# Performance work log

Hardware: AMD Instinct MI355X
Metric: run time of the kernel (lower is better)

The kernel has to match this reference:

```python
import jax, jax.numpy as jnp
import numpy as np

N = 100000        # nodes
E = 1600000       # edges (avg in-degree 16)
D_IN = 128
H = 4             # num_heads
D = 16            # out_feats per head
NEG_SLOPE = 0.2


def setup_inputs() -> dict:
    key = jax.random.key(0)
    k1, k2, k3, k4, k5 = jax.random.split(key, 5)
    feat = jax.random.normal(k1, (N, D_IN), dtype=jnp.float32)
    src = jax.random.randint(k2, (E,), 0, N, dtype=jnp.int32)
    dst = jax.random.randint(k3, (E,), 0, N, dtype=jnp.int32)
    # learned parameters (xavier-ish scale)
    W = jax.random.normal(k4, (H * D, D_IN), dtype=jnp.float32) * (2.0 / np.sqrt(D_IN + H * D))
    attn_weights = jax.random.normal(k5, (2 * H * D,), dtype=jnp.float32) * 0.1
    bias = jnp.zeros((H * D,), dtype=jnp.float32)
    return {"feat": feat, "src": src, "dst": dst, "W": W,
            "attn_weights": attn_weights, "bias": bias}


def reference(feat, src, dst, W, attn_weights, bias):
    # linear projection: [N, H*D] -> [N, H, D]
    z = (feat @ W.T).reshape(N, H, D)
    a = attn_weights.reshape(2, H, D)
    # per-node attention logits for source/destination roles: [N, H]
    el = jnp.einsum('nhd,hd->nh', z, a[0])
    er = jnp.einsum('nhd,hd->nh', z, a[1])
    # per-edge logits + LeakyReLU: [E, H]
    e = jax.nn.leaky_relu(el[src] + er[dst], NEG_SLOPE)
    # segment softmax over incoming edges of each destination node
    m = jax.ops.segment_max(e, dst, num_segments=N)        # [N, H]
    m = jnp.where(jnp.isfinite(m), m, 0.0)                 # guard isolated nodes
    ex = jnp.exp(e - m[dst])                               # [E, H]
    denom = jax.ops.segment_sum(ex, dst, num_segments=N)   # [N, H]
    denom = jnp.where(denom > 0, denom, 1.0)
    alpha = ex / denom[dst]                                # [E, H]
    # weighted scatter-aggregate: out[dst] += alpha * z[src]
    out = jax.ops.segment_sum(alpha[:, :, None] * z[src], dst, num_segments=N)
    return out + bias.reshape(H, D)
```

## Files before the change

### kernel.cpp

```cpp
#include <hip/hip_runtime.h>
#include <hip/hip_fp16.h>
#include <math.h>

#define NUM_H 4
#define HD 64
#define DIN 128
#define NEG_SLOPE 0.2f
#define LOG2E 1.4426950408889634f

#define NBK 128
#define BSH 10
#define NCH 256
#define SRCB 17

typedef _Float16 half8 __attribute__((ext_vector_type(8)));
typedef float f32x4 __attribute__((ext_vector_type(4)));

__device__ inline half8 pack8(float4 a, float4 b) {
  half8 h;
  h[0] = (_Float16)a.x; h[1] = (_Float16)a.y;
  h[2] = (_Float16)a.z; h[3] = (_Float16)a.w;
  h[4] = (_Float16)b.x; h[5] = (_Float16)b.y;
  h[6] = (_Float16)b.z; h[7] = (_Float16)b.w;
  return h;
}

__global__ __launch_bounds__(256) void k_proj(
    const float* __restrict__ feat, const float* __restrict__ Wm,
    const float* __restrict__ attn, __half* __restrict__ zh,
    float* __restrict__ el, float* __restrict__ er, int n) {
  const int lane = threadIdx.x & 63;
  const int wv = threadIdx.x >> 6;
  const int l15 = lane & 15;
  const int g = lane >> 4;
  const int base = blockIdx.x * 64 + wv * 16;

  half8 bf[4][4];
#pragma unroll
  for (int j = 0; j < 4; ++j) {
    const float* wp = Wm + (j * 16 + l15) * 128 + g * 8;
#pragma unroll
    for (int kt = 0; kt < 4; ++kt) {
      float4 w0 = *(const float4*)(wp + kt * 32);
      float4 w1 = *(const float4*)(wp + kt * 32 + 4);
      bf[kt][j] = pack8(w0, w1);
    }
  }

  int arow = base + l15;
  if (arow > n - 1) arow = n - 1;
  const float* fp = feat + (size_t)arow * 128 + g * 8;
  half8 af[4];
#pragma unroll
  for (int kt = 0; kt < 4; ++kt) {
    float4 a0 = *(const float4*)(fp + kt * 32);
    float4 a1 = *(const float4*)(fp + kt * 32 + 4);
    af[kt] = pack8(a0, a1);
  }

  f32x4 acc[4] = {{0.f,0.f,0.f,0.f},{0.f,0.f,0.f,0.f},
                  {0.f,0.f,0.f,0.f},{0.f,0.f,0.f,0.f}};
#pragma unroll
  for (int kt = 0; kt < 4; ++kt)
#pragma unroll
    for (int j = 0; j < 4; ++j)
      acc[j] = __builtin_amdgcn_mfma_f32_16x16x32_f16(af[kt], bf[kt][j], acc[j], 0, 0, 0);

  float a0v[4], a1v[4];
#pragma unroll
  for (int j = 0; j < 4; ++j) {
    a0v[j] = attn[j * 16 + l15];
    a1v[j] = attn[64 + j * 16 + l15];
  }
#pragma unroll
  for (int r = 0; r < 4; ++r) {
    int row = base + g * 4 + r;
    bool ok = row < n;
#pragma unroll
    for (int j = 0; j < 4; ++j) {
      float v = acc[j][r];
      if (ok) zh[(size_t)row * 64 + j * 16 + l15] = __float2half_rn(v);
      float pl = v * a0v[j];
      float pr = v * a1v[j];
#pragma unroll
      for (int o = 8; o >= 1; o >>= 1) {
        pl += __shfl_xor(pl, o, 16);
        pr += __shfl_xor(pr, o, 16);
      }
      if (ok && l15 == 0) {
        el[row * 4 + j] = pl * LOG2E;
        er[row * 4 + j] = pr * LOG2E;
      }
    }
  }
}

__global__ __launch_bounds__(256) void k_hist(const int* __restrict__ dst,
                                              int* __restrict__ mat, int e) {
  __shared__ int h[NBK];
  for (int i = threadIdx.x; i < NBK; i += 256) h[i] = 0;
  __syncthreads();
  const int chunk = (e + NCH - 1) / NCH;
  const int lo = blockIdx.x * chunk;
  const int hi = min(e, lo + chunk);
  const int lo4 = min(hi, (lo + 3) & ~3);
  const int hi4 = (hi & ~3) < lo4 ? lo4 : (hi & ~3);
  for (int i = lo + threadIdx.x; i < lo4; i += 256)
    atomicAdd(&h[dst[i] >> BSH], 1);
  for (int i = lo4 + threadIdx.x * 4; i < hi4; i += 1024) {
    int4 d4 = *reinterpret_cast<const int4*>(dst + i);
    atomicAdd(&h[d4.x >> BSH], 1);
    atomicAdd(&h[d4.y >> BSH], 1);
    atomicAdd(&h[d4.z >> BSH], 1);
    atomicAdd(&h[d4.w >> BSH], 1);
  }
  for (int i = hi4 + threadIdx.x; i < hi; i += 256)
    atomicAdd(&h[dst[i] >> BSH], 1);
  __syncthreads();
  for (int i = threadIdx.x; i < NBK; i += 256)
    mat[blockIdx.x * NBK + i] = h[i];
}

__global__ __launch_bounds__(1024) void k_scanb(int* __restrict__ mat,
                                                int* __restrict__ segpre,
                                                int* __restrict__ bbase,
                                                int* __restrict__ offs,
                                                int e, int n) {
  __shared__ int part[8][NBK];
  __shared__ int tot[NBK];
  const int t = threadIdx.x;
  const int b = t & (NBK - 1);
  const int seg = t >> 7;
  int run = 0;
  for (int c = seg * 32; c < seg * 32 + 32; ++c) {
    int v = mat[c * NBK + b];
    mat[c * NBK + b] = run;
    run += v;
  }
  part[seg][b] = run;
  __syncthreads();
  int mytot = 0;
  if (t < NBK) {
    int acc = 0;
#pragma unroll
    for (int s2 = 0; s2 < 8; ++s2) {
      segpre[s2 * NBK + b] = acc;
      acc += part[s2][b];
    }
    tot[b] = acc;
    mytot = acc;
  }
  __syncthreads();
  for (int off = 1; off < NBK; off <<= 1) {
    int x = 0;
    if (t < NBK && b >= off) x = tot[b - off];
    __syncthreads();
    if (t < NBK) tot[b] += x;
    __syncthreads();
  }
  if (t < NBK) {
    bbase[t] = tot[t] - mytot;
    if (t == NBK - 1) bbase[NBK] = tot[t];
    if (t == 0) offs[n] = e;
  }
}

__global__ __launch_bounds__(256) void k_bucket(
    const int* __restrict__ src, const int* __restrict__ dst,
    const int* __restrict__ mat, const int* __restrict__ segpre,
    const int* __restrict__ bbase, int* __restrict__ bkt, int e) {
  __shared__ int cur[NBK];
  const int seg = blockIdx.x >> 5;
  for (int i = threadIdx.x; i < NBK; i += 256)
    cur[i] = bbase[i] + segpre[seg * NBK + i] + mat[blockIdx.x * NBK + i];
  __syncthreads();
  const int chunk = (e + NCH - 1) / NCH;
  const int lo = blockIdx.x * chunk;
  const int hi = min(e, lo + chunk);
  const int lo4 = min(hi, (lo + 3) & ~3);
  const int hi4 = (hi & ~3) < lo4 ? lo4 : (hi & ~3);
  for (int i = lo + threadIdx.x; i < lo4; i += 256) {
    int d = dst[i];
    int p = atomicAdd(&cur[d >> BSH], 1);
    bkt[p] = ((d & ((1 << BSH) - 1)) << SRCB) | src[i];
  }
  for (int i = lo4 + threadIdx.x * 4; i < hi4; i += 1024) {
    int4 d4 = *reinterpret_cast<const int4*>(dst + i);
    int4 s4 = *reinterpret_cast<const int4*>(src + i);
    int p0 = atomicAdd(&cur[d4.x >> BSH], 1);
    bkt[p0] = ((d4.x & ((1 << BSH) - 1)) << SRCB) | s4.x;
    int p1 = atomicAdd(&cur[d4.y >> BSH], 1);
    bkt[p1] = ((d4.y & ((1 << BSH) - 1)) << SRCB) | s4.y;
    int p2 = atomicAdd(&cur[d4.z >> BSH], 1);
    bkt[p2] = ((d4.z & ((1 << BSH) - 1)) << SRCB) | s4.z;
    int p3 = atomicAdd(&cur[d4.w >> BSH], 1);
    bkt[p3] = ((d4.w & ((1 << BSH) - 1)) << SRCB) | s4.w;
  }
  for (int i = hi4 + threadIdx.x; i < hi; i += 256) {
    int d = dst[i];
    int p = atomicAdd(&cur[d >> BSH], 1);
    bkt[p] = ((d & ((1 << BSH) - 1)) << SRCB) | src[i];
  }
}

__global__ __launch_bounds__(256) void k_csr(
    const int* __restrict__ bkt, const int* __restrict__ bbase,
    int* __restrict__ offs, int* __restrict__ csr, int n) {
  __shared__ int h[1 << BSH];
  __shared__ int wsum[256];
  const int b = blockIdx.x;
  const int base = bbase[b];
  const int cnt = bbase[b + 1] - base;
  const int nlo = b << BSH;
  const int t = threadIdx.x;

  for (int i = t; i < (1 << BSH); i += 256) h[i] = 0;
  __syncthreads();
  for (int i = t; i < cnt; i += 256)
    atomicAdd(&h[bkt[base + i] >> SRCB], 1);
  __syncthreads();

  int v0 = h[t * 4], v1 = h[t * 4 + 1], v2 = h[t * 4 + 2], v3 = h[t * 4 + 3];
  int s = v0 + v1 + v2 + v3;
  wsum[t] = s;
  __syncthreads();
  for (int off = 1; off < 256; off <<= 1) {
    int x = (t >= off) ? wsum[t - off] : 0;
    __syncthreads();
    wsum[t] += x;
    __syncthreads();
  }
  int e0 = wsum[t] - s;
  int e1 = e0 + v0, e2 = e1 + v1, e3 = e2 + v2;
  h[t * 4] = e0; h[t * 4 + 1] = e1; h[t * 4 + 2] = e2; h[t * 4 + 3] = e3;
#pragma unroll
  for (int i = 0; i < 4; ++i) {
    int node = nlo + t * 4 + i;
    int ex = (i == 0) ? e0 : (i == 1) ? e1 : (i == 2) ? e2 : e3;
    if (node < n) offs[node] = base + ex;
  }
  __syncthreads();
  for (int i = t; i < cnt; i += 256) {
    int v = bkt[base + i];
    int p = atomicAdd(&h[v >> SRCB], 1);
    csr[base + p] = v & ((1 << SRCB) - 1);
  }
}

__global__ __launch_bounds__(256) void k_gat(
    const __half2* __restrict__ zh, const float* __restrict__ el,
    const float* __restrict__ er, const int* __restrict__ offs,
    const int* __restrict__ csr, const float* __restrict__ bias,
    float* __restrict__ out, int n, int nwaves) {
  const int lane = threadIdx.x & 63;
  const int h = lane >> 4;
  const int slot = (lane >> 3) & 1;
  const int dp = lane & 7;
  const int gw = (blockIdx.x * 256 + threadIdx.x) >> 6;

  const float2 b2 = reinterpret_cast<const float2*>(bias)[h * 8 + dp];

  for (int node = gw; node < n; node += nwaves) {
    const int beg = offs[node], end = offs[node + 1];
    const float erh = er[node * 4 + h];
    float den = 0.f, ax = 0.f, ay = 0.f;

    int pb = beg;
    for (; pb + 8 <= end; pb += 8) {
      int q = pb + slot;
      int s0 = csr[q];
      int s1 = csr[q + 2];
      int s2 = csr[q + 4];
      int s3 = csr[q + 6];
      float x0 = el[s0 * 4 + h] + erh;
      float x1 = el[s1 * 4 + h] + erh;
      float x2 = el[s2 * 4 + h] + erh;
      float x3 = el[s3 * 4 + h] + erh;
      x0 = fmaxf(x0, x0 * NEG_SLOPE);
      x1 = fmaxf(x1, x1 * NEG_SLOPE);
      x2 = fmaxf(x2, x2 * NEG_SLOPE);
      x3 = fmaxf(x3, x3 * NEG_SLOPE);
      float e0 = exp2f(x0);
      float e1 = exp2f(x1);
      float e2 = exp2f(x2);
      float e3 = exp2f(x3);
      float2 z0 = __half22float2(zh[s0 * 32 + h * 8 + dp]);
      float2 z1 = __half22float2(zh[s1 * 32 + h * 8 + dp]);
      float2 z2 = __half22float2(zh[s2 * 32 + h * 8 + dp]);
      float2 z3 = __half22float2(zh[s3 * 32 + h * 8 + dp]);
      den += e0 + e1 + e2 + e3;
      ax += e0 * z0.x + e1 * z1.x + e2 * z2.x + e3 * z3.x;
      ay += e0 * z0.y + e1 * z1.y + e2 * z2.y + e3 * z3.y;
    }
    for (int q = pb + slot; q < end; q += 2) {
      int s0 = csr[q];
      float x0 = el[s0 * 4 + h] + erh;
      x0 = fmaxf(x0, x0 * NEG_SLOPE);
      float e0 = exp2f(x0);
      float2 z0 = __half22float2(zh[s0 * 32 + h * 8 + dp]);
      den += e0;
      ax += e0 * z0.x;
      ay += e0 * z0.y;
    }

    den += __shfl_xor(den, 8);
    ax += __shfl_xor(ax, 8);
    ay += __shfl_xor(ay, 8);
    if (slot == 0) {
      float d = den <= 0.f ? 1.f : den;
      float inv = 1.f / d;
      float2 o2 = make_float2(ax * inv + b2.x, ay * inv + b2.y);
      reinterpret_cast<float2*>(out)[node * 32 + h * 8 + dp] = o2;
    }
  }
}

extern "C" void kernel_launch(void* const* d_in, const int* in_sizes, int n_in,
                              void* d_out, int out_size, void* d_ws, size_t ws_size,
                              hipStream_t stream) {
  const float* feat = (const float*)d_in[0];
  const int* src = (const int*)d_in[1];
  const int* dst = (const int*)d_in[2];
  const float* Wm = (const float*)d_in[3];
  const float* attn = (const float*)d_in[4];
  const float* bias = (const float*)d_in[5];
  const int n = in_sizes[0] / DIN;
  const int e = in_sizes[1];
  float* out = (float*)d_out;

  __half* zh = (__half*)d_ws;
  int* bkt = (int*)(zh + (size_t)n * HD);
  float* el = (float*)(bkt + e);
  float* er = el + (size_t)n * NUM_H;
  int* offs = (int*)(er + (size_t)n * NUM_H);
  int* csr = offs + (n + 1);
  int* mat = csr + e;
  int* segpre = mat + NCH * NBK;
  int* bbase = segpre + 8 * NBK;

  k_proj<<<(n + 63) / 64, 256, 0, stream>>>(feat, Wm, attn, zh, el, er, n);
  k_hist<<<NCH, 256, 0, stream>>>(dst, mat, e);
  k_scanb<<<1, 1024, 0, stream>>>(mat, segpre, bbase, offs, e, n);
  k_bucket<<<NCH, 256, 0, stream>>>(src, dst, mat, segpre, bbase, bkt, e);
  int nbuckets = (n + (1 << BSH) - 1) >> BSH;
  k_csr<<<nbuckets, 256, 0, stream>>>(bkt, bbase, offs, csr, n);
  const int GB = 2048;
  k_gat<<<GB, 256, 0, stream>>>((const __half2*)zh, el, er, offs, csr, bias,
                                out, n, GB * 4);
}
```

Baseline: 155.5 us.

## Fuse projection into bucket kernel and use finer dst buckets

Merges the MFMA projection kernel with the edge-bucketing kernel in one launch, with block ranges picking the role, so the two independent stages overlap and one launch is dropped. The bucket count rises from 128 to 512 (256 nodes per bucket), so each CSR block handles one node per thread and its scan is simpler, with more blocks for parallelism. The two-level scan uses 2 segments instead of 8, and exp2f becomes the hardware builtin. Risks are a longer serial scan per thread in k_scanb and more shared-memory atomic contention per bucket.

```diff
diff --git a/kernel.cpp b/kernel.cpp
--- a/kernel.cpp
+++ b/kernel.cpp
@@ -8,9 +8,11 @@
 #define NEG_SLOPE 0.2f
 #define LOG2E 1.4426950408889634f
 
-#define NBK 128
-#define BSH 10
+#define NBK 512
+#define BSH 8
 #define NCH 256
+#define SEGS 2
+#define CPS (NCH / SEGS)
 #define SRCB 17
 
 typedef _Float16 half8 __attribute__((ext_vector_type(8)));
@@ -23,76 +25,6 @@
   h[4] = (_Float16)b.x; h[5] = (_Float16)b.y;
   h[6] = (_Float16)b.z; h[7] = (_Float16)b.w;
   return h;
-}
-
-__global__ __launch_bounds__(256) void k_proj(
-    const float* __restrict__ feat, const float* __restrict__ Wm,
-    const float* __restrict__ attn, __half* __restrict__ zh,
-    float* __restrict__ el, float* __restrict__ er, int n) {
-  const int lane = threadIdx.x & 63;
-  const int wv = threadIdx.x >> 6;
-  const int l15 = lane & 15;
-  const int g = lane >> 4;
-  const int base = blockIdx.x * 64 + wv * 16;
-
-  half8 bf[4][4];
-#pragma unroll
-  for (int j = 0; j < 4; ++j) {
-    const float* wp = Wm + (j * 16 + l15) * 128 + g * 8;
-#pragma unroll
-    for (int kt = 0; kt < 4; ++kt) {
-      float4 w0 = *(const float4*)(wp + kt * 32);
-      float4 w1 = *(const float4*)(wp + kt * 32 + 4);
-      bf[kt][j] = pack8(w0, w1);
-    }
-  }
-
-  int arow = base + l15;
-  if (arow > n - 1) arow = n - 1;
-  const float* fp = feat + (size_t)arow * 128 + g * 8;
-  half8 af[4];
-#pragma unroll
-  for (int kt = 0; kt < 4; ++kt) {
-    float4 a0 = *(const float4*)(fp + kt * 32);
-    float4 a1 = *(const float4*)(fp + kt * 32 + 4);
-    af[kt] = pack8(a0, a1);
-  }
-
-  f32x4 acc[4] = {{0.f,0.f,0.f,0.f},{0.f,0.f,0.f,0.f},
-                  {0.f,0.f,0.f,0.f},{0.f,0.f,0.f,0.f}};
-#pragma unroll
-  for (int kt = 0; kt < 4; ++kt)
-#pragma unroll
-    for (int j = 0; j < 4; ++j)
-      acc[j] = __builtin_amdgcn_mfma_f32_16x16x32_f16(af[kt], bf[kt][j], acc[j], 0, 0, 0);
-
-  float a0v[4], a1v[4];
-#pragma unroll
-  for (int j = 0; j < 4; ++j) {
-    a0v[j] = attn[j * 16 + l15];
-    a1v[j] = attn[64 + j * 16 + l15];
-  }
-#pragma unroll
-  for (int r = 0; r < 4; ++r) {
-    int row = base + g * 4 + r;
-    bool ok = row < n;
-#pragma unroll
-    for (int j = 0; j < 4; ++j) {
-      float v = acc[j][r];
-      if (ok) zh[(size_t)row * 64 + j * 16 + l15] = __float2half_rn(v);
-      float pl = v * a0v[j];
-      float pr = v * a1v[j];
-#pragma unroll
-      for (int o = 8; o >= 1; o >>= 1) {
-        pl += __shfl_xor(pl, o, 16);
-        pr += __shfl_xor(pr, o, 16);
-      }
-      if (ok && l15 == 0) {
-        el[row * 4 + j] = pl * LOG2E;
-        er[row * 4 + j] = pr * LOG2E;
-      }
-    }
-  }
 }
 
 __global__ __launch_bounds__(256) void k_hist(const int* __restrict__ dst,
@@ -126,13 +58,13 @@
                                                 int* __restrict__ bbase,
                                                 int* __restrict__ offs,
                                                 int e, int n) {
-  __shared__ int part[8][NBK];
+  __shared__ int part[SEGS][NBK];
   __shared__ int tot[NBK];
   const int t = threadIdx.x;
   const int b = t & (NBK - 1);
-  const int seg = t >> 7;
+  const int seg = t >> 9;
   int run = 0;
-  for (int c = seg * 32; c < seg * 32 + 32; ++c) {
+  for (int c = seg * CPS; c < seg * CPS + CPS; ++c) {
     int v = mat[c * NBK + b];
     mat[c * NBK + b] = run;
     run += v;
@@ -143,7 +75,7 @@
   if (t < NBK) {
     int acc = 0;
 #pragma unroll
-    for (int s2 = 0; s2 < 8; ++s2) {
+    for (int s2 = 0; s2 < SEGS; ++s2) {
       segpre[s2 * NBK + b] = acc;
       acc += part[s2][b];
     }
@@ -165,41 +97,114 @@
   }
 }
 
-__global__ __launch_bounds__(256) void k_bucket(
-    const int* __restrict__ src, const int* __restrict__ dst,
-    const int* __restrict__ mat, const int* __restrict__ segpre,
-    const int* __restrict__ bbase, int* __restrict__ bkt, int e) {
+__global__ __launch_bounds__(256) void k_proj_bucket(
+    const float* __restrict__ feat, const float* __restrict__ Wm,
+    const float* __restrict__ attn, const int* __restrict__ src,
+    const int* __restrict__ dst, const int* __restrict__ mat,
+    const int* __restrict__ segpre, const int* __restrict__ bbase,
+    __half* __restrict__ zh, float* __restrict__ el, float* __restrict__ er,
+    int* __restrict__ bkt, int n, int e) {
   __shared__ int cur[NBK];
-  const int seg = blockIdx.x >> 5;
-  for (int i = threadIdx.x; i < NBK; i += 256)
-    cur[i] = bbase[i] + segpre[seg * NBK + i] + mat[blockIdx.x * NBK + i];
-  __syncthreads();
-  const int chunk = (e + NCH - 1) / NCH;
-  const int lo = blockIdx.x * chunk;
-  const int hi = min(e, lo + chunk);
-  const int lo4 = min(hi, (lo + 3) & ~3);
-  const int hi4 = (hi & ~3) < lo4 ? lo4 : (hi & ~3);
-  for (int i = lo + threadIdx.x; i < lo4; i += 256) {
-    int d = dst[i];
-    int p = atomicAdd(&cur[d >> BSH], 1);
-    bkt[p] = ((d & ((1 << BSH) - 1)) << SRCB) | src[i];
-  }
-  for (int i = lo4 + threadIdx.x * 4; i < hi4; i += 1024) {
-    int4 d4 = *reinterpret_cast<const int4*>(dst + i);
-    int4 s4 = *reinterpret_cast<const int4*>(src + i);
-    int p0 = atomicAdd(&cur[d4.x >> BSH], 1);
-    bkt[p0] = ((d4.x & ((1 << BSH) - 1)) << SRCB) | s4.x;
-    int p1 = atomicAdd(&cur[d4.y >> BSH], 1);
-    bkt[p1] = ((d4.y & ((1 << BSH) - 1)) << SRCB) | s4.y;
-    int p2 = atomicAdd(&cur[d4.z >> BSH], 1);
-    bkt[p2] = ((d4.z & ((1 << BSH) - 1)) << SRCB) | s4.z;
-    int p3 = atomicAdd(&cur[d4.w >> BSH], 1);
-    bkt[p3] = ((d4.w & ((1 << BSH) - 1)) << SRCB) | s4.w;
-  }
-  for (int i = hi4 + threadIdx.x; i < hi; i += 256) {
-    int d = dst[i];
-    int p = atomicAdd(&cur[d >> BSH], 1);
-    bkt[p] = ((d & ((1 << BSH) - 1)) << SRCB) | src[i];
+  if ((int)blockIdx.x < NCH) {
+    const int cb = blockIdx.x;
+    const int seg = cb / CPS;
+    for (int i = threadIdx.x; i < NBK; i += 256)
+      cur[i] = bbase[i] + segpre[seg * NBK + i] + mat[cb * NBK + i];
+    __syncthreads();
+    const int chunk = (e + NCH - 1) / NCH;
+    const int lo = cb * chunk;
+    const int hi = min(e, lo + chunk);
+    const int lo4 = min(hi, (lo + 3) & ~3);
+    const int hi4 = (hi & ~3) < lo4 ? lo4 : (hi & ~3);
+    for (int i = lo + threadIdx.x; i < lo4; i += 256) {
+      int d = dst[i];
+      int p = atomicAdd(&cur[d >> BSH], 1);
+      bkt[p] = ((d & ((1 << BSH) - 1)) << SRCB) | src[i];
+    }
+    for (int i = lo4 + threadIdx.x * 4; i < hi4; i += 1024) {
+      int4 d4 = *reinterpret_cast<const int4*>(dst + i);
+      int4 s4 = *reinterpret_cast<const int4*>(src + i);
+      int p0 = atomicAdd(&cur[d4.x >> BSH], 1);
+      bkt[p0] = ((d4.x & ((1 << BSH) - 1)) << SRCB) | s4.x;
+      int p1 = atomicAdd(&cur[d4.y >> BSH], 1);
+      bkt[p1] = ((d4.y & ((1 << BSH) - 1)) << SRCB) | s4.y;
+      int p2 = atomicAdd(&cur[d4.z >> BSH], 1);
+      bkt[p2] = ((d4.z & ((1 << BSH) - 1)) << SRCB) | s4.z;
+      int p3 = atomicAdd(&cur[d4.w >> BSH], 1);
+      bkt[p3] = ((d4.w & ((1 << BSH) - 1)) << SRCB) | s4.w;
+    }
+    for (int i = hi4 + threadIdx.x; i < hi; i += 256) {
+      int d = dst[i];
+      int p = atomicAdd(&cur[d >> BSH], 1);
+      bkt[p] = ((d & ((1 << BSH) - 1)) << SRCB) | src[i];
+    }
+    return;
+  }
+
+  const int pb = (int)blockIdx.x - NCH;
+  const int lane = threadIdx.x & 63;
+  const int wv = threadIdx.x >> 6;
+  const int l15 = lane & 15;
+  const int g = lane >> 4;
+  const int base = pb * 64 + wv * 16;
+
+  half8 bf[4][4];
+#pragma unroll
+  for (int j = 0; j < 4; ++j) {
+    const float* wp = Wm + (j * 16 + l15) * 128 + g * 8;
+#pragma unroll
+    for (int kt = 0; kt < 4; ++kt) {
+      float4 w0 = *(const float4*)(wp + kt * 32);
+      float4 w1 = *(const float4*)(wp + kt * 32 + 4);
+      bf[kt][j] = pack8(w0, w1);
+    }
+  }
+
+  int arow = base + l15;
+  if (arow > n - 1) arow = n - 1;
+  const float* fp = feat + (size_t)arow * 128 + g * 8;
+  half8 af[4];
+#pragma unroll
+  for (int kt = 0; kt < 4; ++kt) {
+    float4 a0 = *(const float4*)(fp + kt * 32);
+    float4 a1 = *(const float4*)(fp + kt * 32 + 4);
+    af[kt] = pack8(a0, a1);
+  }
+
+  f32x4 acc[4] = {{0.f,0.f,0.f,0.f},{0.f,0.f,0.f,0.f},
+                  {0.f,0.f,0.f,0.f},{0.f,0.f,0.f,0.f}};
+#pragma unroll
+  for (int kt = 0; kt < 4; ++kt)
+#pragma unroll
+    for (int j = 0; j < 4; ++j)
+      acc[j] = __builtin_amdgcn_mfma_f32_16x16x32_f16(af[kt], bf[kt][j], acc[j], 0, 0, 0);
+
+  float a0v[4], a1v[4];
+#pragma unroll
+  for (int j = 0; j < 4; ++j) {
+    a0v[j] = attn[j * 16 + l15];
+    a1v[j] = attn[64 + j * 16 + l15];
+  }
+#pragma unroll
+  for (int r = 0; r < 4; ++r) {
+    int row = base + g * 4 + r;
+    bool ok = row < n;
+#pragma unroll
+    for (int j = 0; j < 4; ++j) {
+      float v = acc[j][r];
+      if (ok) zh[(size_t)row * 64 + j * 16 + l15] = __float2half_rn(v);
+      float pl = v * a0v[j];
+      float pr = v * a1v[j];
+#pragma unroll
+      for (int o = 8; o >= 1; o >>= 1) {
+        pl += __shfl_xor(pl, o, 16);
+        pr += __shfl_xor(pr, o, 16);
+      }
+      if (ok && l15 == 0) {
+        el[row * 4 + j] = pl * LOG2E;
+        er[row * 4 + j] = pr * LOG2E;
+      }
+    }
   }
 }
 
@@ -207,43 +212,36 @@
     const int* __restrict__ bkt, const int* __restrict__ bbase,
     int* __restrict__ offs, int* __restrict__ csr, int n) {
   __shared__ int h[1 << BSH];
-  __shared__ int wsum[256];
+  __shared__ int pre[1 << BSH];
   const int b = blockIdx.x;
   const int base = bbase[b];
   const int cnt = bbase[b + 1] - base;
   const int nlo = b << BSH;
   const int t = threadIdx.x;
 
-  for (int i = t; i < (1 << BSH); i += 256) h[i] = 0;
+  h[t] = 0;
   __syncthreads();
   for (int i = t; i < cnt; i += 256)
     atomicAdd(&h[bkt[base + i] >> SRCB], 1);
   __syncthreads();
 
-  int v0 = h[t * 4], v1 = h[t * 4 + 1], v2 = h[t * 4 + 2], v3 = h[t * 4 + 3];
-  int s = v0 + v1 + v2 + v3;
-  wsum[t] = s;
+  int v = h[t];
+  pre[t] = v;
   __syncthreads();
   for (int off = 1; off < 256; off <<= 1) {
-    int x = (t >= off) ? wsum[t - off] : 0;
-    __syncthreads();
-    wsum[t] += x;
-    __syncthreads();
-  }
-  int e0 = wsum[t] - s;
-  int e1 = e0 + v0, e2 = e1 + v1, e3 = e2 + v2;
-  h[t * 4] = e0; h[t * 4 + 1] = e1; h[t * 4 + 2] = e2; h[t * 4 + 3] = e3;
-#pragma unroll
-  for (int i = 0; i < 4; ++i) {
-    int node = nlo + t * 4 + i;
-    int ex = (i == 0) ? e0 : (i == 1) ? e1 : (i == 2) ? e2 : e3;
-    if (node < n) offs[node] = base + ex;
-  }
+    int x = (t >= off) ? pre[t - off] : 0;
+    __syncthreads();
+    pre[t] += x;
+    __syncthreads();
+  }
+  int excl = pre[t] - v;
+  if (nlo + t < n) offs[nlo + t] = base + excl;
+  h[t] = excl;
   __syncthreads();
   for (int i = t; i < cnt; i += 256) {
-    int v = bkt[base + i];
-    int p = atomicAdd(&h[v >> SRCB], 1);
-    csr[base + p] = v & ((1 << SRCB) - 1);
+    int w = bkt[base + i];
+    int p = atomicAdd(&h[w >> SRCB], 1);
+    csr[base + p] = w & ((1 << SRCB) - 1);
   }
 }
 
@@ -280,10 +278,10 @@
       x1 = fmaxf(x1, x1 * NEG_SLOPE);
       x2 = fmaxf(x2, x2 * NEG_SLOPE);
       x3 = fmaxf(x3, x3 * NEG_SLOPE);
-      float e0 = exp2f(x0);
-      float e1 = exp2f(x1);
-      float e2 = exp2f(x2);
-      float e3 = exp2f(x3);
+      float e0 = __builtin_amdgcn_exp2f(x0);
+      float e1 = __builtin_amdgcn_exp2f(x1);
+      float e2 = __builtin_amdgcn_exp2f(x2);
+      float e3 = __builtin_amdgcn_exp2f(x3);
       float2 z0 = __half22float2(zh[s0 * 32 + h * 8 + dp]);
       float2 z1 = __half22float2(zh[s1 * 32 + h * 8 + dp]);
       float2 z2 = __half22float2(zh[s2 * 32 + h * 8 + dp]);
@@ -296,7 +294,7 @@
       int s0 = csr[q];
       float x0 = el[s0 * 4 + h] + erh;
       x0 = fmaxf(x0, x0 * NEG_SLOPE);
-      float e0 = exp2f(x0);
+      float e0 = __builtin_amdgcn_exp2f(x0);
       float2 z0 = __half22float2(zh[s0 * 32 + h * 8 + dp]);
       den += e0;
       ax += e0 * z0.x;
@@ -336,12 +334,14 @@
   int* csr = offs + (n + 1);
   int* mat = csr + e;
   int* segpre = mat + NCH * NBK;
-  int* bbase = segpre + 8 * NBK;
-
-  k_proj<<<(n + 63) / 64, 256, 0, stream>>>(feat, Wm, attn, zh, el, er, n);
+  int* bbase = segpre + SEGS * NBK;
+
+  const int PB = (n + 63) / 64;
   k_hist<<<NCH, 256, 0, stream>>>(dst, mat, e);
   k_scanb<<<1, 1024, 0, stream>>>(mat, segpre, bbase, offs, e, n);
-  k_bucket<<<NCH, 256, 0, stream>>>(src, dst, mat, segpre, bbase, bkt, e);
+  k_proj_bucket<<<NCH + PB, 256, 0, stream>>>(feat, Wm, attn, src, dst, mat,
+                                              segpre, bbase, zh, el, er, bkt,
+                                              n, e);
   int nbuckets = (n + (1 << BSH) - 1) >> BSH;
   k_csr<<<nbuckets, 256, 0, stream>>>(bkt, bbase, offs, csr, n);
   const int GB = 2048;
```

Measured after the change: 141.8 us. 8.8% less time.
